# Kernel optimization log

Hardware: AMD Instinct MI355X
Metric: run time of the kernel (lower is better)

The kernel has to match this reference:

```python
import jax, jax.numpy as jnp
import numpy as np

N_FEAT = 1024
NEG_INF = -1e30  # stand-in for -inf that is safe in fp32 softmax


def setup_inputs() -> dict:
    key = jax.random.key(0)
    k1, k2 = jax.random.split(key)
    T, C = 4096, N_FEAT
    x = jax.random.normal(k1, (T, C), dtype=jnp.float32)
    W = jax.random.normal(k2, (C, 3 * C), dtype=jnp.float32) * (1.0 / np.sqrt(C))
    b = jnp.zeros((3 * C,), dtype=jnp.float32)
    return {"x": x, "W": W, "b": b, "n_padd": 0}


def reference(x, W, b, n_padd):
    T, C = x.shape
    qkv = x @ W + b                      # [T, 3C]
    q, k, v = jnp.split(qkv, 3, axis=1)  # each [T, C]
    att = (q @ k.T) * (1.0 / jnp.sqrt(jnp.float32(C)))  # [T, T]
    idx = jnp.arange(T)
    # causal mask AND padding mask: only keys >= n_padd for queries >= n_padd
    mask = (idx[None, :] <= idx[:, None]) & (idx[None, :] >= n_padd) & (idx[:, None] >= n_padd)
    att = jnp.where(mask, att, NEG_INF)
    att = jax.nn.softmax(att, axis=-1)
    y = att @ v                          # [T, C]
    return y
```

## Files before the change

### kernel.cpp

```cpp
#include <hip/hip_runtime.h>
#include <hip/hip_bf16.h>
#include <math.h>

#define C_DIM 1024
#define QKS  2048
#define BM   128
#define BN   64
#define BK   32

typedef __attribute__((ext_vector_type(8))) short bf16x8;
typedef __attribute__((ext_vector_type(4))) float f32x4;

__device__ __forceinline__ unsigned short f2bf(float f) {
  __hip_bfloat16 h = __float2bfloat16(f);
  return *(reinterpret_cast<unsigned short*>(&h));
}
__device__ __forceinline__ float bf2f(unsigned short u) {
  return __uint_as_float(((unsigned int)u) << 16);
}
__device__ __forceinline__ f32x4 mfma16(bf16x8 a, bf16x8 b, f32x4 c) {
  return __builtin_amdgcn_mfma_f32_16x16x32_bf16(a, b, c, 0, 0, 0);
}

__device__ __forceinline__ void gload_lds16(const unsigned short* g,
                                            unsigned short* l) {
  __builtin_amdgcn_global_load_lds(
      (const __attribute__((address_space(1))) void*)(g),
      (__attribute__((address_space(3))) void*)(l), 16, 0, 0);
}

__global__ __launch_bounds__(256) void cast_x(
    const float* __restrict__ x, unsigned short* __restrict__ xb) {
  const int i = (blockIdx.x * 256 + threadIdx.x) << 2;
  float4 v = *(const float4*)(x + i);
  ushort4 u;
  u.x = f2bf(v.x); u.y = f2bf(v.y); u.z = f2bf(v.z); u.w = f2bf(v.w);
  *(ushort4*)(xb + i) = u;
}

__global__ __launch_bounds__(256) void transpose_w(
    const float* __restrict__ W, unsigned short* __restrict__ WT) {
  __shared__ float Ls[64][65];
  const int n0 = blockIdx.x * 64;
  const int k0 = blockIdx.y * 64;
  const int c = (threadIdx.x & 15) << 2;
  const int r = threadIdx.x >> 4;
#pragma unroll
  for (int rr = 0; rr < 64; rr += 16) {
    float4 v = *(const float4*)(W + (size_t)(k0 + r + rr) * 3072 + n0 + c);
    Ls[r + rr][c + 0] = v.x; Ls[r + rr][c + 1] = v.y;
    Ls[r + rr][c + 2] = v.z; Ls[r + rr][c + 3] = v.w;
  }
  __syncthreads();
#pragma unroll
  for (int rr = 0; rr < 64; rr += 16) {
    const int X = r + rr;
    ushort4 u;
    u.x = f2bf(Ls[c + 0][X]); u.y = f2bf(Ls[c + 1][X]);
    u.z = f2bf(Ls[c + 2][X]); u.w = f2bf(Ls[c + 3][X]);
    *(ushort4*)(WT + (size_t)(n0 + X) * C_DIM + k0 + c) = u;
  }
}

template <int MODE>
__global__ __launch_bounds__(256) void gemm64(
    const unsigned short* __restrict__ A_, const unsigned short* __restrict__ BT_,
    void* __restrict__ Cv, const float* __restrict__ bias_,
    int lda, int ldb, int ldc, int T) {
  __shared__ __align__(16) unsigned short As[2][BM][BK];
  __shared__ __align__(16) unsigned short Bs[2][BN][BK];

  const int tid = threadIdx.x, lane = tid & 63, w = tid >> 6;
  const int qd = lane >> 4, n16 = lane & 15;

  const unsigned short* A  = A_;
  const unsigned short* BT = BT_;
  const float* bias = bias_;
  unsigned short* Cb = (unsigned short*)Cv;
  float* Cf = (float*)Cv;
  int ldc_ = ldc;
  int m0, n0, kbeg = 0, kend = C_DIM;
  bool use_atomic = false;
  bool rowbias = false;

  if (MODE == 4) {
    const int nQKx = QKS / BN;
    const int nQK  = (T >> 7) * nQKx;
    int id = (int)blockIdx.x;
    if (id < nQK) {
      m0 = (id / nQKx) * BM; n0 = (id % nQKx) * BN;
    } else {
      id -= nQK;
      const int nVx = T / BN;
      m0 = (id / nVx) * BM; n0 = (id % nVx) * BN;
      A  = BT_ + (size_t)QKS * C_DIM;
      BT = A_;
      Cb = (unsigned short*)Cv + (size_t)T * QKS;
      bias = bias_ + QKS;
      rowbias = true;
      ldc_ = T;
    }
  } else if (MODE == 2) {
    if ((int)(blockIdx.x >> 1) > (int)blockIdx.y) return;
    m0 = blockIdx.y * BM; n0 = blockIdx.x * BN;
  } else {
    const int nyt = T >> 7;
    const int ex  = nyt > 16 ? nyt - 16 : 0;
    const int by  = (int)blockIdx.y;
    int bi, seg;
    if (by < nyt) { bi = by; seg = 0; } else { bi = by - ex; seg = 1; }
    const int kc = (bi + 1) << 7;
    kbeg = seg ? 2048 : 0;
    kend = seg ? kc : (kc < 2048 ? kc : 2048);
    m0 = bi << 7; n0 = blockIdx.x * BN;
    use_atomic = (kc > 2048);
  }

  f32x4 s[2][4];
#pragma unroll
  for (int mt = 0; mt < 2; ++mt)
#pragma unroll
    for (int nn = 0; nn < 4; ++nn) s[mt][nn] = (f32x4){0.f, 0.f, 0.f, 0.f};

  const int srow = lane >> 2;
  const int skc  = (lane & 3) << 3;
  const unsigned short* ag0 = A  + (size_t)(m0 + (w << 5) + srow)      * lda + kbeg + skc;
  const unsigned short* ag1 = A  + (size_t)(m0 + (w << 5) + 16 + srow) * lda + kbeg + skc;
  const unsigned short* bg0 = BT + (size_t)(n0 + (w << 4) + srow)      * ldb + kbeg + skc;

  const int ntiles = (kend - kbeg) >> 5;

  gload_lds16(ag0, &As[0][(w << 5)][0]);
  gload_lds16(ag1, &As[0][(w << 5) + 16][0]);
  gload_lds16(bg0, &Bs[0][(w << 4)][0]);

  int cur = 0;
  for (int t = 0; t < ntiles; ++t) {
    __syncthreads();
    if (t + 1 < ntiles) {
      const int ko = (t + 1) << 5;
      const int nb = cur ^ 1;
      gload_lds16(ag0 + ko, &As[nb][(w << 5)][0]);
      gload_lds16(ag1 + ko, &As[nb][(w << 5) + 16][0]);
      gload_lds16(bg0 + ko, &Bs[nb][(w << 4)][0]);
    }
    bf16x8 bf[4];
#pragma unroll
    for (int nn = 0; nn < 4; ++nn)
      bf[nn] = *(const bf16x8*)&Bs[cur][(nn << 4) + n16][qd << 3];
#pragma unroll
    for (int mt = 0; mt < 2; ++mt) {
      bf16x8 af = *(const bf16x8*)&As[cur][(w << 5) + (mt << 4) + n16][qd << 3];
#pragma unroll
      for (int nn = 0; nn < 4; ++nn)
        s[mt][nn] = mfma16(af, bf[nn], s[mt][nn]);
    }
    cur ^= 1;
  }

  if (MODE == 3) {
#pragma unroll
    for (int mt = 0; mt < 2; ++mt)
#pragma unroll
      for (int nn = 0; nn < 4; ++nn) {
        const int col = n0 + (nn << 4) + n16;
#pragma unroll
        for (int r = 0; r < 4; ++r) {
          const int row = m0 + (w << 5) + (mt << 4) + (qd << 2) + r;
          if (use_atomic) atomicAdd(&Cf[(size_t)row * ldc_ + col], s[mt][nn][r]);
          else            Cf[(size_t)row * ldc_ + col] = s[mt][nn][r];
        }
      }
  } else {
#pragma unroll
    for (int mt = 0; mt < 2; ++mt)
#pragma unroll
      for (int nn = 0; nn < 4; ++nn) {
        const int col = n0 + (nn << 4) + n16;
        const float bc = (MODE == 4 && !rowbias) ? bias[col] : 0.f;
#pragma unroll
        for (int r = 0; r < 4; ++r) {
          const int row = m0 + (w << 5) + (mt << 4) + (qd << 2) + r;
          float v = s[mt][nn][r];
          if (MODE == 4) v += rowbias ? bias[row] : bc;
          if (MODE == 2) v *= 0.03125f;
          Cb[(size_t)row * ldc_ + col] = f2bf(v);
        }
      }
  }
}

__global__ __launch_bounds__(256) void softmax_rows(
    unsigned short* __restrict__ P, const int* __restrict__ np_p, int T) {
  __shared__ float red[8];
  const int i = blockIdx.x;
  const int np = *np_p;
  const int klen = ((i >> 7) + 1) << 7;
  const int tid = threadIdx.x, lane = tid & 63, w = tid >> 6;
  const int j0 = tid << 4;
  unsigned short* rowp = P + (size_t)i * T;
  const bool act = j0 < klen;

  if (i < np) {
    if (act) {
      uint4 z = {0, 0, 0, 0};
      *(uint4*)(rowp + j0) = z;
      *(uint4*)(rowp + j0 + 8) = z;
    }
    return;
  }

  float v[16];
  float mx = -3.0e38f;
  if (act) {
    uint4 u0 = *(const uint4*)(rowp + j0);
    uint4 u1 = *(const uint4*)(rowp + j0 + 8);
    const unsigned int uu[8] = {u0.x, u0.y, u0.z, u0.w, u1.x, u1.y, u1.z, u1.w};
#pragma unroll
    for (int u = 0; u < 8; ++u) {
      v[2 * u]     = bf2f(uu[u] & 0xffff);
      v[2 * u + 1] = bf2f(uu[u] >> 16);
    }
#pragma unroll
    for (int u = 0; u < 16; ++u) {
      const int j = j0 + u;
      if (j > i || j < np) v[u] = -3.0e38f;
      mx = fmaxf(mx, v[u]);
    }
  }
  mx = fmaxf(mx, __shfl_xor(mx, 32));
  mx = fmaxf(mx, __shfl_xor(mx, 16));
  mx = fmaxf(mx, __shfl_xor(mx, 8));
  mx = fmaxf(mx, __shfl_xor(mx, 4));
  mx = fmaxf(mx, __shfl_xor(mx, 2));
  mx = fmaxf(mx, __shfl_xor(mx, 1));
  if (lane == 0) red[w] = mx;
  __syncthreads();
  const float M = fmaxf(fmaxf(red[0], red[1]), fmaxf(red[2], red[3]));

  float sum = 0.f;
  if (act) {
#pragma unroll
    for (int u = 0; u < 16; ++u) {
      const float p = (v[u] > -1.0e30f) ? __expf(v[u] - M) : 0.f;
      v[u] = p;
      sum += p;
    }
  }
  sum += __shfl_xor(sum, 32);
  sum += __shfl_xor(sum, 16);
  sum += __shfl_xor(sum, 8);
  sum += __shfl_xor(sum, 4);
  sum += __shfl_xor(sum, 2);
  sum += __shfl_xor(sum, 1);
  if (lane == 0) red[4 + w] = sum;
  __syncthreads();
  const float inv = 1.0f / (red[4] + red[5] + red[6] + red[7]);

  if (act) {
    unsigned int o[8];
#pragma unroll
    for (int u = 0; u < 8; ++u) {
      const unsigned int lo = f2bf(v[2 * u] * inv);
      const unsigned int hi = f2bf(v[2 * u + 1] * inv);
      o[u] = lo | (hi << 16);
    }
    uint4 s0 = {o[0], o[1], o[2], o[3]};
    uint4 s1 = {o[4], o[5], o[6], o[7]};
    *(uint4*)(rowp + j0) = s0;
    *(uint4*)(rowp + j0 + 8) = s1;
  }
}

__global__ __launch_bounds__(256) void zero_hi(float* __restrict__ out) {
  const size_t i = ((size_t)blockIdx.x * 256 + threadIdx.x) * 4 +
                   (size_t)2048 * C_DIM;
  float4 z = {0.f, 0.f, 0.f, 0.f};
  *(float4*)(out + i) = z;
}

__global__ __launch_bounds__(256) void padfix(
    const unsigned short* __restrict__ vtb, const int* __restrict__ np_p,
    float* __restrict__ out, int T) {
  const int np = *np_p;
  const int row0 = blockIdx.x * 32;
  if (row0 >= np) return;
  const int pc = min(np - row0, 32);
  const int c4 = threadIdx.x << 2;
  float a[4] = {0.f, 0.f, 0.f, 0.f};
#pragma unroll
  for (int c = 0; c < 4; ++c) {
    const unsigned short* vr = vtb + (size_t)(c4 + c) * T;
    for (int j = 0; j < T; j += 8) {
      uint4 v = *(const uint4*)(vr + j);
      a[c] += bf2f(v.x & 0xffff) + bf2f(v.x >> 16) + bf2f(v.y & 0xffff) + bf2f(v.y >> 16)
            + bf2f(v.z & 0xffff) + bf2f(v.z >> 16) + bf2f(v.w & 0xffff) + bf2f(v.w >> 16);
    }
  }
  const float inv = 1.0f / (float)T;
  float4 rv = {a[0] * inv, a[1] * inv, a[2] * inv, a[3] * inv};
  for (int r = 0; r < pc; ++r)
    *(float4*)(out + (size_t)(row0 + r) * C_DIM + c4) = rv;
}

extern "C" void kernel_launch(void* const* d_in, const int* in_sizes, int n_in,
                              void* d_out, int out_size, void* d_ws, size_t ws_size,
                              hipStream_t stream) {
  const float* x    = (const float*)d_in[0];
  const float* W    = (const float*)d_in[1];
  const float* b    = (const float*)d_in[2];
  const int* n_padd = (const int*)d_in[3];
  float* out = (float*)d_out;

  const int T = in_sizes[0] / C_DIM;
  unsigned short* qkb = (unsigned short*)d_ws;
  unsigned short* vtb = qkb + (size_t)T * QKS;
  unsigned short* xb  = vtb + (size_t)C_DIM * T;
  unsigned short* WT  = xb  + (size_t)T * C_DIM;
  unsigned short* P   = xb;

  cast_x<<<(T * C_DIM) / 1024, 256, 0, stream>>>(x, xb);
  transpose_w<<<dim3(48, 16), 256, 0, stream>>>(W, WT);

  {
    const int nQK = (T / BM) * (QKS / BN);
    const int nV  = (C_DIM / BM) * (T / BN);
    gemm64<4><<<nQK + nV, 256, 0, stream>>>(
        xb, WT, qkb, b, C_DIM, C_DIM, QKS, T);
  }
  gemm64<2><<<dim3(T / BN, T / BM), 256, 0, stream>>>(
      qkb, qkb + C_DIM, P, b, QKS, QKS, T, T);
  softmax_rows<<<T, 256, 0, stream>>>(P, n_padd, T);
  zero_hi<<<((T - 2048) * C_DIM) / 1024, 256, 0, stream>>>(out);
  {
    const int nyt = T / BM;
    const int ex = nyt > 16 ? nyt - 16 : 0;
    gemm64<3><<<dim3(C_DIM / BN, nyt + ex), 256, 0, stream>>>(
        P, vtb, out, b, T, T, C_DIM, T);
  }
  padfix<<<T / 32, 256, 0, stream>>>(vtb, n_padd, out, T);
}
```

Before: 241.5 us.

## Replace 128x64 GEMM with 256x256 tile, 8-wave, swizzled LDS pipelined kernel

Replaces the small 128x64x32 GEMM with a 256x256x64 tile kernel using 8 waves, XOR-swizzled LDS layout, explicit vmcnt/barrier pipelining with split staging across four MFMA quads, and raised priority around MFMAs. The causal split-K in the PV GEMM is re-derived for 256-row tiles with 1024-wide K segments and atomics, and softmax/zero_hi are adjusted to the new tile granularity. The aim is higher arithmetic intensity and better MFMA utilization. In exchange there are fewer blocks, causing coarser causal masking waste and heavier register pressure.

Result: faster. 224.1 us (-7.2%).

```diff
diff --git a/kernel.cpp b/kernel.cpp
--- a/kernel.cpp
+++ b/kernel.cpp
@@ -4,9 +4,6 @@
 
 #define C_DIM 1024
 #define QKS  2048
-#define BM   128
-#define BN   64
-#define BK   32
 
 typedef __attribute__((ext_vector_type(8))) short bf16x8;
 typedef __attribute__((ext_vector_type(4))) float f32x4;
@@ -21,13 +18,17 @@
 __device__ __forceinline__ f32x4 mfma16(bf16x8 a, bf16x8 b, f32x4 c) {
   return __builtin_amdgcn_mfma_f32_16x16x32_bf16(a, b, c, 0, 0, 0);
 }
-
 __device__ __forceinline__ void gload_lds16(const unsigned short* g,
                                             unsigned short* l) {
   __builtin_amdgcn_global_load_lds(
       (const __attribute__((address_space(1))) void*)(g),
       (__attribute__((address_space(3))) void*)(l), 16, 0, 0);
 }
+
+#define VMCNT(n)  asm volatile("s_waitcnt vmcnt(" #n ")" ::: "memory")
+#define LGKMCNT0  asm volatile("s_waitcnt lgkmcnt(0)" ::: "memory")
+#define SBAR      __builtin_amdgcn_sched_barrier(0)
+#define BARRIER   __builtin_amdgcn_s_barrier()
 
 __global__ __launch_bounds__(256) void cast_x(
     const float* __restrict__ x, unsigned short* __restrict__ xb) {
@@ -63,14 +64,15 @@
 }
 
 template <int MODE>
-__global__ __launch_bounds__(256) void gemm64(
+__global__ __launch_bounds__(512) void gemm256(
     const unsigned short* __restrict__ A_, const unsigned short* __restrict__ BT_,
     void* __restrict__ Cv, const float* __restrict__ bias_,
     int lda, int ldb, int ldc, int T) {
-  __shared__ __align__(16) unsigned short As[2][BM][BK];
-  __shared__ __align__(16) unsigned short Bs[2][BN][BK];
+  __shared__ __align__(16) unsigned short As[2][2][128][64];
+  __shared__ __align__(16) unsigned short Bs[2][2][128][64];
 
   const int tid = threadIdx.x, lane = tid & 63, w = tid >> 6;
+  const int wr = w >> 2, wc = w & 3;
   const int qd = lane >> 4, n16 = lane & 15;
 
   const unsigned short* A  = A_;
@@ -80,114 +82,163 @@
   float* Cf = (float*)Cv;
   int ldc_ = ldc;
   int m0, n0, kbeg = 0, kend = C_DIM;
-  bool use_atomic = false;
-  bool rowbias = false;
+  bool use_atomic = false, rowbias = false;
 
   if (MODE == 4) {
-    const int nQKx = QKS / BN;
-    const int nQK  = (T >> 7) * nQKx;
+    const int nQKx = QKS >> 8;
+    const int nQK  = (T >> 8) * nQKx;
     int id = (int)blockIdx.x;
     if (id < nQK) {
-      m0 = (id / nQKx) * BM; n0 = (id % nQKx) * BN;
+      m0 = (id / nQKx) << 8; n0 = (id % nQKx) << 8;
     } else {
       id -= nQK;
-      const int nVx = T / BN;
-      m0 = (id / nVx) * BM; n0 = (id % nVx) * BN;
+      const int nVx = T >> 8;
+      m0 = (id / nVx) << 8; n0 = (id % nVx) << 8;
       A  = BT_ + (size_t)QKS * C_DIM;
       BT = A_;
       Cb = (unsigned short*)Cv + (size_t)T * QKS;
-      bias = bias_ + QKS;
-      rowbias = true;
-      ldc_ = T;
+      bias = bias_ + QKS; rowbias = true; ldc_ = T;
     }
   } else if (MODE == 2) {
-    if ((int)(blockIdx.x >> 1) > (int)blockIdx.y) return;
-    m0 = blockIdx.y * BM; n0 = blockIdx.x * BN;
+    if ((int)blockIdx.x > (int)blockIdx.y) return;
+    m0 = (int)blockIdx.y << 8; n0 = (int)blockIdx.x << 8;
   } else {
-    const int nyt = T >> 7;
-    const int ex  = nyt > 16 ? nyt - 16 : 0;
-    const int by  = (int)blockIdx.y;
-    int bi, seg;
-    if (by < nyt) { bi = by; seg = 0; } else { bi = by - ex; seg = 1; }
-    const int kc = (bi + 1) << 7;
-    kbeg = seg ? 2048 : 0;
-    kend = seg ? kc : (kc < 2048 ? kc : 2048);
-    m0 = bi << 7; n0 = blockIdx.x * BN;
-    use_atomic = (kc > 2048);
-  }
-
-  f32x4 s[2][4];
-#pragma unroll
-  for (int mt = 0; mt < 2; ++mt)
-#pragma unroll
-    for (int nn = 0; nn < 4; ++nn) s[mt][nn] = (f32x4){0.f, 0.f, 0.f, 0.f};
-
-  const int srow = lane >> 2;
-  const int skc  = (lane & 3) << 3;
-  const unsigned short* ag0 = A  + (size_t)(m0 + (w << 5) + srow)      * lda + kbeg + skc;
-  const unsigned short* ag1 = A  + (size_t)(m0 + (w << 5) + 16 + srow) * lda + kbeg + skc;
-  const unsigned short* bg0 = BT + (size_t)(n0 + (w << 4) + srow)      * ldb + kbeg + skc;
-
-  const int ntiles = (kend - kbeg) >> 5;
-
-  gload_lds16(ag0, &As[0][(w << 5)][0]);
-  gload_lds16(ag1, &As[0][(w << 5) + 16][0]);
-  gload_lds16(bg0, &Bs[0][(w << 4)][0]);
-
-  int cur = 0;
-  for (int t = 0; t < ntiles; ++t) {
-    __syncthreads();
-    if (t + 1 < ntiles) {
-      const int ko = (t + 1) << 5;
-      const int nb = cur ^ 1;
-      gload_lds16(ag0 + ko, &As[nb][(w << 5)][0]);
-      gload_lds16(ag1 + ko, &As[nb][(w << 5) + 16][0]);
-      gload_lds16(bg0 + ko, &Bs[nb][(w << 4)][0]);
-    }
-    bf16x8 bf[4];
-#pragma unroll
-    for (int nn = 0; nn < 4; ++nn)
-      bf[nn] = *(const bf16x8*)&Bs[cur][(nn << 4) + n16][qd << 3];
-#pragma unroll
-    for (int mt = 0; mt < 2; ++mt) {
-      bf16x8 af = *(const bf16x8*)&As[cur][(w << 5) + (mt << 4) + n16][qd << 3];
-#pragma unroll
-      for (int nn = 0; nn < 4; ++nn)
-        s[mt][nn] = mfma16(af, bf[nn], s[mt][nn]);
-    }
-    cur ^= 1;
+    const int nnx = C_DIM >> 8;
+    int id = (int)blockIdx.x;
+    const int nx = id % nnx;
+    int s = id / nnx;
+    int bi = 0;
+    while (s >= ((bi >> 2) + 1)) { s -= (bi >> 2) + 1; ++bi; }
+    m0 = bi << 8; n0 = nx << 8;
+    kbeg = s << 10;
+    const int kfull = (bi + 1) << 8;
+    kend = kbeg + 1024 < kfull ? kbeg + 1024 : kfull;
+    use_atomic = (kfull > 1024);
+  }
+
+  const int NT = (kend - kbeg) >> 6;
+
+  const int l3 = lane >> 3;
+  const int su = (((lane & 7) ^ l3) << 3);
+  const unsigned short* asrc[2][2];
+  const unsigned short* bsrc[2][2];
+#pragma unroll
+  for (int g = 0; g < 2; ++g)
+#pragma unroll
+    for (int c = 0; c < 2; ++c) {
+      asrc[g][c] = A  + (size_t)(m0 + c * 128 + g * 64 + (w << 3) + l3) * lda + kbeg + su;
+      bsrc[g][c] = BT + (size_t)(n0 + (c * 2 + (w >> 2)) * 64 + g * 32 + ((w & 3) << 3) + l3) * ldb + kbeg + su;
+    }
+
+#define STAGE_A(buf, g, kk) do { \
+    gload_lds16(asrc[g][0] + (kk), &As[buf][g][(w << 3)][0]);      \
+    gload_lds16(asrc[g][1] + (kk), &As[buf][g][64 + (w << 3)][0]); \
+  } while (0)
+#define STAGE_B(buf, g, kk) do { \
+    gload_lds16(bsrc[g][0] + (kk), &Bs[buf][g][(w << 3)][0]);      \
+    gload_lds16(bsrc[g][1] + (kk), &Bs[buf][g][64 + (w << 3)][0]); \
+  } while (0)
+
+  const int arow = (wr << 6) + n16;
+  const int brow = (wc << 5) + n16;
+  const int sw0 = ((qd ^ (n16 & 7)) << 3);
+  const int sw1 = (((4 + qd) ^ (n16 & 7)) << 3);
+
+#define READ_A(AA, mh, buf) do { \
+  _Pragma("unroll") for (int fm = 0; fm < 4; ++fm) { \
+    AA[fm][0] = *(const bf16x8*)&As[buf][mh][arow + fm * 16][sw0]; \
+    AA[fm][1] = *(const bf16x8*)&As[buf][mh][arow + fm * 16][sw1]; \
+  } } while (0)
+#define READ_B(BB, g, buf) do { \
+  _Pragma("unroll") for (int fn = 0; fn < 2; ++fn) { \
+    BB[fn][0] = *(const bf16x8*)&Bs[buf][g][brow + fn * 16][sw0]; \
+    BB[fn][1] = *(const bf16x8*)&Bs[buf][g][brow + fn * 16][sw1]; \
+  } } while (0)
+
+  f32x4 acc[8][4];
+#pragma unroll
+  for (int i = 0; i < 8; ++i)
+#pragma unroll
+    for (int j = 0; j < 4; ++j) acc[i][j] = (f32x4){0.f, 0.f, 0.f, 0.f};
+
+#define MFMA_QUAD(mh, nh, AA, BB) do { \
+  _Pragma("unroll") for (int fm = 0; fm < 4; ++fm) \
+  _Pragma("unroll") for (int fn = 0; fn < 2; ++fn) { \
+    acc[(mh) * 4 + fm][(nh) * 2 + fn] = mfma16(AA[fm][0], BB[fn][0], acc[(mh) * 4 + fm][(nh) * 2 + fn]); \
+    acc[(mh) * 4 + fm][(nh) * 2 + fn] = mfma16(AA[fm][1], BB[fn][1], acc[(mh) * 4 + fm][(nh) * 2 + fn]); \
+  } } while (0)
+
+  STAGE_A(0, 0, 0); STAGE_B(0, 0, 0);
+  STAGE_A(0, 1, 0); STAGE_B(0, 1, 0);
+  if (NT > 1) { STAGE_A(1, 0, 64); STAGE_B(1, 0, 64); }
+  if (NT > 1) VMCNT(8); else VMCNT(4);
+  SBAR; BARRIER;
+
+  bf16x8 a[4][2], b0[2][2], b1[2][2];
+  for (int t = 0; t < NT; ++t) {
+    const int p = t & 1, pn = p ^ 1;
+    const int knx  = (t + 1) << 6;
+    const int knx2 = (t + 2) << 6;
+    const bool s1 = (t + 1 < NT), s2 = (t + 2 < NT);
+
+    READ_A(a, 0, p); READ_B(b0, 0, p);
+    if (s1) STAGE_A(pn, 1, knx);
+    if (s1) { VMCNT(6); } else { VMCNT(0); }
+    SBAR; BARRIER; LGKMCNT0; SBAR;
+    __builtin_amdgcn_s_setprio(1); MFMA_QUAD(0, 0, a, b0); __builtin_amdgcn_s_setprio(0);
+    SBAR; BARRIER;
+    READ_B(b1, 1, p);
+    if (s1) STAGE_B(pn, 1, knx);
+    SBAR; BARRIER; LGKMCNT0; SBAR;
+    __builtin_amdgcn_s_setprio(1); MFMA_QUAD(0, 1, a, b1); __builtin_amdgcn_s_setprio(0);
+    SBAR; BARRIER;
+    READ_A(a, 1, p);
+    if (s2) STAGE_A(p, 0, knx2);
+    SBAR; BARRIER; LGKMCNT0; SBAR;
+    __builtin_amdgcn_s_setprio(1); MFMA_QUAD(1, 0, a, b0); __builtin_amdgcn_s_setprio(0);
+    SBAR; BARRIER;
+    if (s2) STAGE_B(p, 0, knx2);
+    if (s1) { if (s2) { VMCNT(8); } else { VMCNT(4); } }
+    SBAR; BARRIER;
+    __builtin_amdgcn_s_setprio(1); MFMA_QUAD(1, 1, a, b1); __builtin_amdgcn_s_setprio(0);
+    SBAR; BARRIER;
   }
 
   if (MODE == 3) {
 #pragma unroll
-    for (int mt = 0; mt < 2; ++mt)
-#pragma unroll
-      for (int nn = 0; nn < 4; ++nn) {
-        const int col = n0 + (nn << 4) + n16;
+    for (int fm = 0; fm < 8; ++fm)
+#pragma unroll
+      for (int fn = 0; fn < 4; ++fn) {
+        const int col  = n0 + (wc << 6) + (fn << 4) + n16;
+        const int rowb = m0 + (wr << 7) + (fm << 4) + (qd << 2);
 #pragma unroll
         for (int r = 0; r < 4; ++r) {
-          const int row = m0 + (w << 5) + (mt << 4) + (qd << 2) + r;
-          if (use_atomic) atomicAdd(&Cf[(size_t)row * ldc_ + col], s[mt][nn][r]);
-          else            Cf[(size_t)row * ldc_ + col] = s[mt][nn][r];
+          if (use_atomic) atomicAdd(&Cf[(size_t)(rowb + r) * ldc_ + col], acc[fm][fn][r]);
+          else            Cf[(size_t)(rowb + r) * ldc_ + col] = acc[fm][fn][r];
         }
       }
   } else {
 #pragma unroll
-    for (int mt = 0; mt < 2; ++mt)
-#pragma unroll
-      for (int nn = 0; nn < 4; ++nn) {
-        const int col = n0 + (nn << 4) + n16;
+    for (int fm = 0; fm < 8; ++fm)
+#pragma unroll
+      for (int fn = 0; fn < 4; ++fn) {
+        const int col  = n0 + (wc << 6) + (fn << 4) + n16;
+        const int rowb = m0 + (wr << 7) + (fm << 4) + (qd << 2);
         const float bc = (MODE == 4 && !rowbias) ? bias[col] : 0.f;
 #pragma unroll
         for (int r = 0; r < 4; ++r) {
-          const int row = m0 + (w << 5) + (mt << 4) + (qd << 2) + r;
-          float v = s[mt][nn][r];
-          if (MODE == 4) v += rowbias ? bias[row] : bc;
+          float v = acc[fm][fn][r];
+          if (MODE == 4) v += rowbias ? bias[rowb + r] : bc;
           if (MODE == 2) v *= 0.03125f;
-          Cb[(size_t)row * ldc_ + col] = f2bf(v);
+          Cb[(size_t)(rowb + r) * ldc_ + col] = f2bf(v);
         }
       }
   }
+#undef STAGE_A
+#undef STAGE_B
+#undef READ_A
+#undef READ_B
+#undef MFMA_QUAD
 }
 
 __global__ __launch_bounds__(256) void softmax_rows(
@@ -195,7 +246,7 @@
   __shared__ float red[8];
   const int i = blockIdx.x;
   const int np = *np_p;
-  const int klen = ((i >> 7) + 1) << 7;
+  const int klen = ((i >> 8) + 1) << 8;
   const int tid = threadIdx.x, lane = tid & 63, w = tid >> 6;
   const int j0 = tid << 4;
   unsigned short* rowp = P + (size_t)i * T;
@@ -274,7 +325,7 @@
 
 __global__ __launch_bounds__(256) void zero_hi(float* __restrict__ out) {
   const size_t i = ((size_t)blockIdx.x * 256 + threadIdx.x) * 4 +
-                   (size_t)2048 * C_DIM;
+                   (size_t)1024 * C_DIM;
   float4 z = {0.f, 0.f, 0.f, 0.f};
   *(float4*)(out + i) = z;
 }
@@ -323,19 +374,20 @@
   transpose_w<<<dim3(48, 16), 256, 0, stream>>>(W, WT);
 
   {
-    const int nQK = (T / BM) * (QKS / BN);
-    const int nV  = (C_DIM / BM) * (T / BN);
-    gemm64<4><<<nQK + nV, 256, 0, stream>>>(
+    const int nQK = (T >> 8) * (QKS >> 8);
+    const int nV  = (C_DIM >> 8) * (T >> 8);
+    gemm256<4><<<nQK + nV, 512, 0, stream>>>(
         xb, WT, qkb, b, C_DIM, C_DIM, QKS, T);
   }
-  gemm64<2><<<dim3(T / BN, T / BM), 256, 0, stream>>>(
+  gemm256<2><<<dim3(T >> 8, T >> 8), 512, 0, stream>>>(
       qkb, qkb + C_DIM, P, b, QKS, QKS, T, T);
   softmax_rows<<<T, 256, 0, stream>>>(P, n_padd, T);
-  zero_hi<<<((T - 2048) * C_DIM) / 1024, 256, 0, stream>>>(out);
+  zero_hi<<<((T - 1024) * C_DIM) / 1024, 256, 0, stream>>>(out);
   {
-    const int nyt = T / BM;
-    const int ex = nyt > 16 ? nyt - 16 : 0;
-    gemm64<3><<<dim3(C_DIM / BN, nyt + ex), 256, 0, stream>>>(
+    const int nyt = T >> 8;
+    int slots = 0;
+    for (int bi = 0; bi < nyt; ++bi) slots += (bi >> 2) + 1;
+    gemm256<3><<<slots * (C_DIM >> 8), 512, 0, stream>>>(
         P, vtb, out, b, T, T, C_DIM, T);
   }
   padfix<<<T / 32, 256, 0, stream>>>(vtb, n_padd, out, T);
```
